# Optimization experiments

Measured on AMD Instinct MI355X. Metric: run time of the kernel, lower is better.

The kernel has to match this reference:

```python
import jax, jax.numpy as jnp
import numpy as np

B, N, F, E = 2, 50000, 128, 500000


def setup_inputs() -> dict:
    key = jax.random.key(0)
    ks = jax.random.split(key, 7)
    x0 = jax.random.normal(ks[0], (B, N, F), dtype=jnp.float32)
    dst = jax.random.randint(ks[1], (E,), 0, N, dtype=jnp.int32)
    src = jax.random.randint(ks[2], (E,), 0, N, dtype=jnp.int32)
    # torch Linear weights: [out_features, in_features]
    w0 = jax.random.normal(ks[3], (F, 2 * F), dtype=jnp.float32) * 0.05
    b0 = jax.random.normal(ks[4], (F,), dtype=jnp.float32) * 0.05
    w1 = jax.random.normal(ks[5], (F, F), dtype=jnp.float32) * 0.05
    b1 = jax.random.normal(ks[6], (F,), dtype=jnp.float32) * 0.05
    return {"x0": x0, "dst": dst, "src": src, "w0": w0, "b0": b0, "w1": w1, "b1": b1}


def reference(x0, dst, src, w0, b0, w1, b1):
    n = x0.shape[1]
    # gather source node features per edge: [B, E, F] -> [E, B, F] for segment ops
    xe = jnp.transpose(x0[:, src], (1, 0, 2))
    # scatter-reduce over destination nodes (include_self=False semantics)
    s = jax.ops.segment_sum(xe, dst, num_segments=n)                      # [N, B, F]
    mx = jax.ops.segment_max(xe, dst, num_segments=n)                     # [N, B, F]
    cnt = jax.ops.segment_sum(jnp.ones((dst.shape[0],), x0.dtype), dst, num_segments=n)  # [N]
    has_edge = (cnt > 0)[:, None, None]
    x0t = jnp.transpose(x0, (1, 0, 2))                                    # [N, B, F]
    # nodes with no incoming edges keep their original values
    mean = jnp.where(has_edge, s / jnp.maximum(cnt, 1.0)[:, None, None], x0t)
    amax = jnp.where(has_edge, mx, x0t)
    x = jnp.concatenate([mean, amax], axis=-1)                            # [N, B, 2F]
    h = jax.nn.relu(jnp.einsum('nbf,of->nbo', x, w0) + b0)
    # dropout is identity in eval mode
    out = x0t + jnp.einsum('nbf,of->nbo', h, w1) + b1
    return jnp.transpose(out, (1, 0, 2))                                  # [B, N, F]
```

## Files before the change

kernel.cpp:

```cpp
#include <hip/hip_runtime.h>

#define NN 50000
#define FF 128
constexpr int NBF2 = NN * 256;
constexpr int CAP  = 64;
constexpr int CSTR = 16;

typedef __attribute__((ext_vector_type(4))) short short4v;
typedef __attribute__((ext_vector_type(8))) short short8;
typedef __attribute__((ext_vector_type(4))) float floatx4;

__device__ __forceinline__ unsigned short f2bf(float x) {
    unsigned int u = __float_as_uint(x);
    unsigned int r = (u + 0x7fff + ((u >> 16) & 1)) >> 16;
    return (unsigned short)r;
}
__device__ __forceinline__ float bf2f(short x) {
    return __uint_as_float(((unsigned int)(unsigned short)x) << 16);
}

__global__ __launch_bounds__(256)
void convert_fill(const int* __restrict__ dst, const int* __restrict__ src, int E,
                  const float* __restrict__ x0,
                  const float* __restrict__ w0, const float* __restrict__ w1,
                  int* __restrict__ cursor, unsigned short* __restrict__ esrc,
                  unsigned short* __restrict__ x0b,
                  unsigned short* __restrict__ w0b, unsigned short* __restrict__ w1b) {
    int i = blockIdx.x * 256 + threadIdx.x;
    if (i < E) {
        int d = dst[i];
        int pos = atomicAdd(&cursor[d * CSTR], 1);
        if (pos < CAP) esrc[d * CAP + pos] = (unsigned short)src[i];
    }
    int stride = gridDim.x * 256;
    for (int p = i; p < NBF2 / 4; p += stride) {
        int v0 = p * 4;
        int n = v0 >> 8;
        int b = (v0 >> 7) & 1;
        int f = v0 & 127;
        const float4 in = *(const float4*)&x0[(b * NN + n) * FF + f];
        short4v o = { (short)f2bf(in.x), (short)f2bf(in.y), (short)f2bf(in.z), (short)f2bf(in.w) };
        *(short4v*)&x0b[v0] = o;
    }
    if (i < 128 * 256) w0b[i] = f2bf(w0[i]);
    if (i < 128 * 128) w1b[i] = f2bf(w1[i]);
}

constexpr int NPB = 8;
constexpr int XCP = 256 + 8;
constexpr int HSP = 128 + 8;

__global__ __launch_bounds__(256, 6)
void fused_gcn(const unsigned short* __restrict__ x0b,
               const float* __restrict__ x0,
               const int* __restrict__ deg,
               const unsigned short* __restrict__ esrc,
               const unsigned short* __restrict__ w0b,
               const float* __restrict__ b0,
               const unsigned short* __restrict__ w1b,
               const float* __restrict__ b1,
               float* __restrict__ out) {
    __shared__ unsigned short xc[16 * XCP];
    __shared__ int sl_hs[16 * HSP / 2];
    __shared__ int cum[9];
    int* sl = sl_hs;
    unsigned short* hs = (unsigned short*)sl_hs;

    int t = threadIdx.x;
    int q = t >> 6;
    int l = t & 63;
    int n0 = blockIdx.x * NPB;

    if (t < 8) cum[t + 1] = min(deg[(n0 + t) * CSTR], CAP);
    if (t == 8) cum[0] = 0;
    __syncthreads();
    if (t == 0) {
        int run = 0;
        for (int i = 1; i <= 8; ++i) { run += cum[i]; cum[i] = run; }
    }
    __syncthreads();

    int T = cum[8];
    for (int i = t; i < T + 8; i += 256) {
        if (i < T) {
            int j = 0;
            while (cum[j + 1] <= i) ++j;
            sl[i] = (j << 16) | (int)esrc[(n0 + j) * CAP + (i - cum[j])];
        } else {
            sl[i] = (NPB << 16);
        }
    }
    __syncthreads();

    int l4 = l * 4;
    int bb = l >> 5;
    int ff = (l & 31) * 4;
    const float NEG_INF = __int_as_float(0xFF800000);

    int jb = q * 2;
    int nb = n0 + jb;
    int eS = __builtin_amdgcn_readfirstlane(cum[jb]);
    int eE = __builtin_amdgcn_readfirstlane(cum[jb + 2]);

    float sA0=0,sA1=0,sA2=0,sA3=0, sB0=0,sB1=0,sB2=0,sB3=0;
    float mA0=NEG_INF,mA1=NEG_INF,mA2=NEG_INF,mA3=NEG_INF;
    float mB0=NEG_INF,mB1=NEG_INF,mB2=NEG_INF,mB3=NEG_INF;

#define GATH_K(k) \
    int u##k = __builtin_amdgcn_readfirstlane(sl[e + k]); \
    short4v r##k = *(const short4v*)&x0b[((u##k & 0xffff) << 8) + l4];

#define ACC_K(k) { \
    int ja = u##k >> 16; \
    if ((ja >> 1) == q) { \
        float v0=bf2f(r##k[0]), v1=bf2f(r##k[1]), v2=bf2f(r##k[2]), v3=bf2f(r##k[3]); \
        if ((ja & 1) == 0) { \
            sA0+=v0; sA1+=v1; sA2+=v2; sA3+=v3; \
            mA0=fmaxf(mA0,v0); mA1=fmaxf(mA1,v1); mA2=fmaxf(mA2,v2); mA3=fmaxf(mA3,v3); \
        } else { \
            sB0+=v0; sB1+=v1; sB2+=v2; sB3+=v3; \
            mB0=fmaxf(mB0,v0); mB1=fmaxf(mB1,v1); mB2=fmaxf(mB2,v2); mB3=fmaxf(mB3,v3); \
        } \
    } }

    for (int e = eS; e < eE; e += 8) {
        GATH_K(0) GATH_K(1) GATH_K(2) GATH_K(3)
        GATH_K(4) GATH_K(5) GATH_K(6) GATH_K(7)
        ACC_K(0) ACC_K(1) ACC_K(2) ACC_K(3)
        ACC_K(4) ACC_K(5) ACC_K(6) ACC_K(7)
    }
#undef GATH_K
#undef ACC_K

#define FINAL_G(g, S0,S1,S2,S3, M0,M1,M2,M3) { \
    int dgx = __builtin_amdgcn_readfirstlane(cum[jb + g + 1] - cum[jb + g]); \
    float me0,me1,me2,me3,a0,a1,a2,a3; \
    if (dgx > 0) { \
        float inv = 1.0f / (float)dgx; \
        me0=S0*inv; me1=S1*inv; me2=S2*inv; me3=S3*inv; \
        a0=M0; a1=M1; a2=M2; a3=M3; \
    } else { \
        short4v rr = *(const short4v*)&x0b[((nb + g) << 8) + l4]; \
        me0=a0=bf2f(rr[0]); me1=a1=bf2f(rr[1]); me2=a2=bf2f(rr[2]); me3=a3=bf2f(rr[3]); \
    } \
    int row = (jb + g) * 2 + bb; \
    short4v mv = { (short)f2bf(me0),(short)f2bf(me1),(short)f2bf(me2),(short)f2bf(me3) }; \
    short4v av = { (short)f2bf(a0),(short)f2bf(a1),(short)f2bf(a2),(short)f2bf(a3) }; \
    *(short4v*)&xc[row * XCP + ff]       = mv; \
    *(short4v*)&xc[row * XCP + 128 + ff] = av; \
}
    FINAL_G(0, sA0,sA1,sA2,sA3, mA0,mA1,mA2,mA3)
    FINAL_G(1, sB0,sB1,sB2,sB3, mB0,mB1,mB2,mB3)
#undef FINAL_G
    __syncthreads();

    int m    = l & 15;
    int quad = l >> 4;
    int colbase = q * 32;

    floatx4 acc[2];
#pragma unroll
    for (int ct = 0; ct < 2; ++ct) acc[ct] = (floatx4){0.f, 0.f, 0.f, 0.f};
#pragma unroll
    for (int ks = 0; ks < 8; ++ks) {
        short8 a = *(const short8*)&xc[m * XCP + ks * 32 + quad * 8];
#pragma unroll
        for (int ct = 0; ct < 2; ++ct) {
            short8 bfr = *(const short8*)&w0b[(colbase + ct * 16 + m) * 256 + ks * 32 + quad * 8];
            acc[ct] = __builtin_amdgcn_mfma_f32_16x16x32_bf16(a, bfr, acc[ct], 0, 0, 0);
        }
    }
#pragma unroll
    for (int ct = 0; ct < 2; ++ct) {
        int col = colbase + ct * 16 + m;
        float bias = b0[col];
#pragma unroll
        for (int r = 0; r < 4; ++r) {
            int row = quad * 4 + r;
            hs[row * HSP + col] = f2bf(fmaxf(acc[ct][r] + bias, 0.0f));
        }
    }
    __syncthreads();

    floatx4 acc2[2];
#pragma unroll
    for (int ct = 0; ct < 2; ++ct) acc2[ct] = (floatx4){0.f, 0.f, 0.f, 0.f};
#pragma unroll
    for (int ks = 0; ks < 4; ++ks) {
        short8 a = *(const short8*)&hs[m * HSP + ks * 32 + quad * 8];
#pragma unroll
        for (int ct = 0; ct < 2; ++ct) {
            short8 bfr = *(const short8*)&w1b[(colbase + ct * 16 + m) * 128 + ks * 32 + quad * 8];
            acc2[ct] = __builtin_amdgcn_mfma_f32_16x16x32_bf16(a, bfr, acc2[ct], 0, 0, 0);
        }
    }
#pragma unroll
    for (int ct = 0; ct < 2; ++ct) {
        int col = colbase + ct * 16 + m;
        float bias = b1[col];
#pragma unroll
        for (int r = 0; r < 4; ++r) {
            int row = quad * 4 + r;
            int n  = n0 + (row >> 1);
            int b2 = row & 1;
            int oi = (b2 * NN + n) * FF + col;
            out[oi] = x0[oi] + bias + acc2[ct][r];
        }
    }
}

extern "C" void kernel_launch(void* const* d_in, const int* in_sizes, int n_in,
                              void* d_out, int out_size, void* d_ws, size_t ws_size,
                              hipStream_t stream) {
    const float* x0  = (const float*)d_in[0];
    const int*   dst = (const int*)d_in[1];
    const int*   src = (const int*)d_in[2];
    const float* w0  = (const float*)d_in[3];
    const float* b0  = (const float*)d_in[4];
    const float* w1  = (const float*)d_in[5];
    const float* b1  = (const float*)d_in[6];
    float* out = (float*)d_out;
    int E = in_sizes[1];

    int* cursor = (int*)d_ws;
    unsigned short* esrc = (unsigned short*)(cursor + (size_t)NN * CSTR);
    unsigned short* x0b  = esrc + (size_t)NN * CAP;
    unsigned short* w0b  = x0b + NBF2;
    unsigned short* w1b  = w0b + 128 * 256;

    int eb = (E + 255) / 256;

    hipMemsetAsync(cursor, 0, (size_t)NN * CSTR * sizeof(int), stream);
    convert_fill<<<eb, 256, 0, stream>>>(dst, src, E, x0, w0, w1, cursor, esrc, x0b, w0b, w1b);
    fused_gcn<<<NN / NPB, 256, 0, stream>>>(x0b, x0, cursor, esrc, w0b, b0, w1b, b1, out);
}
```

Before: 234.6 us.

## Read per-node edge lists directly via readlane, dropping LDS prefix-sum staging

```diff
diff --git a/kernel.cpp b/kernel.cpp
--- a/kernel.cpp
+++ b/kernel.cpp
@@ -50,7 +50,7 @@
 constexpr int XCP = 256 + 8;
 constexpr int HSP = 128 + 8;
 
-__global__ __launch_bounds__(256, 6)
+__global__ __launch_bounds__(256, 8)
 void fused_gcn(const unsigned short* __restrict__ x0b,
                const float* __restrict__ x0,
                const int* __restrict__ deg,
@@ -61,97 +61,86 @@
                const float* __restrict__ b1,
                float* __restrict__ out) {
     __shared__ unsigned short xc[16 * XCP];
-    __shared__ int sl_hs[16 * HSP / 2];
-    __shared__ int cum[9];
-    int* sl = sl_hs;
-    unsigned short* hs = (unsigned short*)sl_hs;
+    __shared__ unsigned short hs[16 * HSP];
 
     int t = threadIdx.x;
     int q = t >> 6;
     int l = t & 63;
     int n0 = blockIdx.x * NPB;
-
-    if (t < 8) cum[t + 1] = min(deg[(n0 + t) * CSTR], CAP);
-    if (t == 8) cum[0] = 0;
-    __syncthreads();
-    if (t == 0) {
-        int run = 0;
-        for (int i = 1; i <= 8; ++i) { run += cum[i]; cum[i] = run; }
-    }
-    __syncthreads();
-
-    int T = cum[8];
-    for (int i = t; i < T + 8; i += 256) {
-        if (i < T) {
-            int j = 0;
-            while (cum[j + 1] <= i) ++j;
-            sl[i] = (j << 16) | (int)esrc[(n0 + j) * CAP + (i - cum[j])];
-        } else {
-            sl[i] = (NPB << 16);
-        }
-    }
-    __syncthreads();
+    int nA = n0 + q * 2;
+    int nB = nA + 1;
 
     int l4 = l * 4;
     int bb = l >> 5;
     int ff = (l & 31) * 4;
     const float NEG_INF = __int_as_float(0xFF800000);
 
-    int jb = q * 2;
-    int nb = n0 + jb;
-    int eS = __builtin_amdgcn_readfirstlane(cum[jb]);
-    int eE = __builtin_amdgcn_readfirstlane(cum[jb + 2]);
+    int vA = esrc[nA * CAP + l];
+    int vB = esrc[nB * CAP + l];
+    int dA = min(__builtin_amdgcn_readfirstlane(deg[nA * CSTR]), CAP);
+    int dB = min(__builtin_amdgcn_readfirstlane(deg[nB * CSTR]), CAP);
 
     float sA0=0,sA1=0,sA2=0,sA3=0, sB0=0,sB1=0,sB2=0,sB3=0;
     float mA0=NEG_INF,mA1=NEG_INF,mA2=NEG_INF,mA3=NEG_INF;
     float mB0=NEG_INF,mB1=NEG_INF,mB2=NEG_INF,mB3=NEG_INF;
 
-#define GATH_K(k) \
-    int u##k = __builtin_amdgcn_readfirstlane(sl[e + k]); \
-    short4v r##k = *(const short4v*)&x0b[((u##k & 0xffff) << 8) + l4];
-
-#define ACC_K(k) { \
-    int ja = u##k >> 16; \
-    if ((ja >> 1) == q) { \
-        float v0=bf2f(r##k[0]), v1=bf2f(r##k[1]), v2=bf2f(r##k[2]), v3=bf2f(r##k[3]); \
-        if ((ja & 1) == 0) { \
-            sA0+=v0; sA1+=v1; sA2+=v2; sA3+=v3; \
-            mA0=fmaxf(mA0,v0); mA1=fmaxf(mA1,v1); mA2=fmaxf(mA2,v2); mA3=fmaxf(mA3,v3); \
-        } else { \
-            sB0+=v0; sB1+=v1; sB2+=v2; sB3+=v3; \
-            mB0=fmaxf(mB0,v0); mB1=fmaxf(mB1,v1); mB2=fmaxf(mB2,v2); mB3=fmaxf(mB3,v3); \
-        } \
-    } }
-
-    for (int e = eS; e < eE; e += 8) {
-        GATH_K(0) GATH_K(1) GATH_K(2) GATH_K(3)
-        GATH_K(4) GATH_K(5) GATH_K(6) GATH_K(7)
-        ACC_K(0) ACC_K(1) ACC_K(2) ACC_K(3)
-        ACC_K(4) ACC_K(5) ACC_K(6) ACC_K(7)
-    }
-#undef GATH_K
-#undef ACC_K
-
-#define FINAL_G(g, S0,S1,S2,S3, M0,M1,M2,M3) { \
-    int dgx = __builtin_amdgcn_readfirstlane(cum[jb + g + 1] - cum[jb + g]); \
+#define ACCV(r, S0,S1,S2,S3, M0,M1,M2,M3) { \
+    float v0=bf2f(r[0]), v1=bf2f(r[1]), v2=bf2f(r[2]), v3=bf2f(r[3]); \
+    S0+=v0; S1+=v1; S2+=v2; S3+=v3; \
+    M0=fmaxf(M0,v0); M1=fmaxf(M1,v1); M2=fmaxf(M2,v2); M3=fmaxf(M3,v3); }
+
+#define GLOOP(vv, dd, S0,S1,S2,S3, M0,M1,M2,M3) \
+    for (int k = 0; k < dd; k += 8) { \
+        int u0 = __builtin_amdgcn_readlane(vv, k + 0); u0 = (u0 < NN) ? u0 : 0; \
+        int u1 = __builtin_amdgcn_readlane(vv, k + 1); u1 = (u1 < NN) ? u1 : 0; \
+        int u2 = __builtin_amdgcn_readlane(vv, k + 2); u2 = (u2 < NN) ? u2 : 0; \
+        int u3 = __builtin_amdgcn_readlane(vv, k + 3); u3 = (u3 < NN) ? u3 : 0; \
+        int u4 = __builtin_amdgcn_readlane(vv, k + 4); u4 = (u4 < NN) ? u4 : 0; \
+        int u5 = __builtin_amdgcn_readlane(vv, k + 5); u5 = (u5 < NN) ? u5 : 0; \
+        int u6 = __builtin_amdgcn_readlane(vv, k + 6); u6 = (u6 < NN) ? u6 : 0; \
+        int u7 = __builtin_amdgcn_readlane(vv, k + 7); u7 = (u7 < NN) ? u7 : 0; \
+        short4v r0 = *(const short4v*)&x0b[(u0 << 8) + l4]; \
+        short4v r1 = *(const short4v*)&x0b[(u1 << 8) + l4]; \
+        short4v r2 = *(const short4v*)&x0b[(u2 << 8) + l4]; \
+        short4v r3 = *(const short4v*)&x0b[(u3 << 8) + l4]; \
+        short4v r4 = *(const short4v*)&x0b[(u4 << 8) + l4]; \
+        short4v r5 = *(const short4v*)&x0b[(u5 << 8) + l4]; \
+        short4v r6 = *(const short4v*)&x0b[(u6 << 8) + l4]; \
+        short4v r7 = *(const short4v*)&x0b[(u7 << 8) + l4]; \
+        ACCV(r0, S0,S1,S2,S3, M0,M1,M2,M3) \
+        if (k + 1 < dd) ACCV(r1, S0,S1,S2,S3, M0,M1,M2,M3) \
+        if (k + 2 < dd) ACCV(r2, S0,S1,S2,S3, M0,M1,M2,M3) \
+        if (k + 3 < dd) ACCV(r3, S0,S1,S2,S3, M0,M1,M2,M3) \
+        if (k + 4 < dd) ACCV(r4, S0,S1,S2,S3, M0,M1,M2,M3) \
+        if (k + 5 < dd) ACCV(r5, S0,S1,S2,S3, M0,M1,M2,M3) \
+        if (k + 6 < dd) ACCV(r6, S0,S1,S2,S3, M0,M1,M2,M3) \
+        if (k + 7 < dd) ACCV(r7, S0,S1,S2,S3, M0,M1,M2,M3) \
+    }
+
+    GLOOP(vA, dA, sA0,sA1,sA2,sA3, mA0,mA1,mA2,mA3)
+    GLOOP(vB, dB, sB0,sB1,sB2,sB3, mB0,mB1,mB2,mB3)
+#undef GLOOP
+#undef ACCV
+
+#define FINAL_N(g, nn, dgx, S0,S1,S2,S3, M0,M1,M2,M3) { \
     float me0,me1,me2,me3,a0,a1,a2,a3; \
     if (dgx > 0) { \
         float inv = 1.0f / (float)dgx; \
         me0=S0*inv; me1=S1*inv; me2=S2*inv; me3=S3*inv; \
         a0=M0; a1=M1; a2=M2; a3=M3; \
     } else { \
-        short4v rr = *(const short4v*)&x0b[((nb + g) << 8) + l4]; \
+        short4v rr = *(const short4v*)&x0b[((nn) << 8) + l4]; \
         me0=a0=bf2f(rr[0]); me1=a1=bf2f(rr[1]); me2=a2=bf2f(rr[2]); me3=a3=bf2f(rr[3]); \
     } \
-    int row = (jb + g) * 2 + bb; \
+    int row = (q * 2 + g) * 2 + bb; \
     short4v mv = { (short)f2bf(me0),(short)f2bf(me1),(short)f2bf(me2),(short)f2bf(me3) }; \
     short4v av = { (short)f2bf(a0),(short)f2bf(a1),(short)f2bf(a2),(short)f2bf(a3) }; \
     *(short4v*)&xc[row * XCP + ff]       = mv; \
     *(short4v*)&xc[row * XCP + 128 + ff] = av; \
 }
-    FINAL_G(0, sA0,sA1,sA2,sA3, mA0,mA1,mA2,mA3)
-    FINAL_G(1, sB0,sB1,sB2,sB3, mB0,mB1,mB2,mB3)
-#undef FINAL_G
+    FINAL_N(0, nA, dA, sA0,sA1,sA2,sA3, mA0,mA1,mA2,mA3)
+    FINAL_N(1, nB, dB, sB0,sB1,sB2,sB3, mB0,mB1,mB2,mB3)
+#undef FINAL_N
     __syncthreads();
 
     int m    = l & 15;
```

Result: slower. 243.2 us (+3.6%).
